# Performance work log

Hardware: AMD Instinct MI355X
Metric: run time of the kernel (lower is better)

## Reference

```python
import jax, jax.numpy as jnp
import numpy as np


def setup_inputs() -> dict:
    key = jax.random.key(0)
    k1, k2, k3, k4 = jax.random.split(key, 4)
    T, H, E, I = 4096, 1024, 8, 3584
    return {
        "hidden_states": jax.random.normal(k1, (T, H), dtype=jnp.float32),
        "gate_w": jax.random.normal(k2, (H, E), dtype=jnp.float32) * 0.02,
        "w1": jax.random.normal(k3, (E, H, I), dtype=jnp.float32) * 0.02,
        "w2": jax.random.normal(k4, (E, I, H), dtype=jnp.float32) * 0.02,
        "top_k": 2,
    }


def reference(hidden_states, gate_w, w1, w2, top_k):
    # Router: logits -> softmax -> top-k -> renormalize (Mixtral / vLLM fused_moe)
    router_logits = hidden_states @ gate_w                    # [T, E]
    probs = jax.nn.softmax(router_logits, axis=-1)
    top_vals, top_idx = jax.lax.top_k(probs, top_k)           # [T, K]
    top_vals = top_vals / jnp.sum(top_vals, axis=-1, keepdims=True)
    E = gate_w.shape[1]
    # Dense per-(token, expert) combine weights, zero for non-selected experts
    dense_w = jnp.sum(jax.nn.one_hot(top_idx, E, dtype=hidden_states.dtype)
                      * top_vals[..., None], axis=1)          # [T, E]
    # Expert MLP: silu(x @ w1[e]) @ w2[e], weighted by routing probs
    act = jax.nn.silu(jnp.einsum('th,ehi->tei', hidden_states, w1))  # [T, E, I]
    act = act * dense_w[:, :, None]
    out = jnp.einsum('tei,eih->th', act, w2)                  # [T, H]
    return out
```

## Files before the change

### kernel.cpp

```cpp
#include <hip/hip_runtime.h>
#include <hip/hip_bf16.h>

#define T_TOK 4096
#define H_DIM 1024
#define E_NUM 8
#define I_DIM 3584
#define NPAIR (T_TOK * 2)
#define MAX_RT 72

#define BM 128
#define BN 128
#define BK 64

typedef __attribute__((ext_vector_type(8))) short bf16x8;
typedef __attribute__((ext_vector_type(4))) float f32x4;
typedef __attribute__((ext_vector_type(8))) unsigned short ushort8_t;
typedef __attribute__((ext_vector_type(4))) unsigned short ushort4_t;

__device__ __forceinline__ unsigned short f2bf(float x) {
  unsigned int u = __float_as_uint(x);
  unsigned int r = (u + 0x7FFFu + ((u >> 16) & 1u)) >> 16;
  return (unsigned short)r;
}

__device__ __forceinline__ void gload16(const void* g, unsigned short* l) {
  __builtin_amdgcn_global_load_lds(
      (const __attribute__((address_space(1))) void*)g,
      (__attribute__((address_space(3))) void*)l, 16, 0, 0);
}

__device__ __forceinline__ void transpose_body(const float* __restrict__ src,
                                               unsigned short* __restrict__ dst,
                                               int R, int C, int e, int c0, int r0,
                                               char* smem) {
  float (*tile)[65] = reinterpret_cast<float (*)[65]>(smem);
  const float* s = src + (size_t)e * R * C;
  unsigned short* d = dst + (size_t)e * R * C;
  const int th = threadIdx.x;
  const int tr = th >> 4;
  const int tc4 = (th & 15) * 4;
#pragma unroll
  for (int it = 0; it < 4; ++it) {
    const int r = it * 16 + tr;
    float4 v = *reinterpret_cast<const float4*>(s + (size_t)(r0 + r) * C + c0 + tc4);
    tile[r][tc4] = v.x; tile[r][tc4 + 1] = v.y; tile[r][tc4 + 2] = v.z; tile[r][tc4 + 3] = v.w;
  }
  __syncthreads();
  const int wc = th >> 3;
  const int wr = (th & 7) * 8;
#pragma unroll
  for (int it = 0; it < 2; ++it) {
    const int c = it * 32 + wc;
    ushort8_t o;
#pragma unroll
    for (int j = 0; j < 8; ++j) o[j] = f2bf(tile[wr + j][c]);
    *reinterpret_cast<ushort8_t*>(d + (size_t)(c0 + c) * R + r0 + wr) = o;
  }
}

__device__ __forceinline__ void router_body(const float* __restrict__ hs,
                                            const float* __restrict__ gw,
                                            unsigned short* __restrict__ hsb,
                                            int* __restrict__ eid, float* __restrict__ wgt,
                                            int* __restrict__ counts, int rbid, char* smem) {
  float* s_gw = reinterpret_cast<float*>(smem);
  int* s_cnt = reinterpret_cast<int*>(smem + 32768);
  const int th = threadIdx.x;
  for (int u = th; u < 2048; u += 256) {
    const f32x4 v = *reinterpret_cast<const f32x4*>(gw + u * 4);
    *reinterpret_cast<f32x4*>(&s_gw[(u ^ ((u >> 3) & 7)) * 4]) = v;
  }
  if (th < E_NUM) s_cnt[th] = 0;
  __syncthreads();

  const int l = th & 63, w = th >> 6;
#pragma unroll 1
  for (int tt = 0; tt < 4; ++tt) {
    const int t = rbid * 16 + w * 4 + tt;
    const float* hrow = hs + (size_t)t * H_DIM;
    unsigned short* brow = hsb + (size_t)t * H_DIM;
    float acc[E_NUM];
#pragma unroll
    for (int e = 0; e < E_NUM; ++e) acc[e] = 0.f;
#pragma unroll
    for (int i = 0; i < 4; ++i) {
      const int h0 = i * 256 + l * 4;
      const f32x4 x = *reinterpret_cast<const f32x4*>(hrow + h0);
      ushort4_t o = { f2bf(x[0]), f2bf(x[1]), f2bf(x[2]), f2bf(x[3]) };
      *reinterpret_cast<ushort4_t*>(brow + h0) = o;
#pragma unroll
      for (int j = 0; j < 4; ++j) {
        const int h = h0 + j;
        const int p0 = (h * 2) ^ ((h >> 2) & 7);
        const f32x4 g0 = *reinterpret_cast<const f32x4*>(&s_gw[p0 * 4]);
        const f32x4 g1 = *reinterpret_cast<const f32x4*>(&s_gw[(p0 ^ 1) * 4]);
        acc[0] += x[j] * g0[0]; acc[1] += x[j] * g0[1];
        acc[2] += x[j] * g0[2]; acc[3] += x[j] * g0[3];
        acc[4] += x[j] * g1[0]; acc[5] += x[j] * g1[1];
        acc[6] += x[j] * g1[2]; acc[7] += x[j] * g1[3];
      }
    }
#pragma unroll
    for (int e = 0; e < E_NUM; ++e) {
#pragma unroll
      for (int off = 1; off < 64; off <<= 1) acc[e] += __shfl_xor(acc[e], off);
    }
    if (l == 0) {
      int i1 = 0;
#pragma unroll
      for (int e = 1; e < E_NUM; ++e) if (acc[e] > acc[i1]) i1 = e;
      int i2 = (i1 == 0) ? 1 : 0;
#pragma unroll
      for (int e = 0; e < E_NUM; ++e) if (e != i1 && acc[e] > acc[i2]) i2 = e;
      const float e2 = __expf(acc[i2] - acc[i1]);
      const float inv = 1.f / (1.f + e2);
      eid[t * 2] = i1;     wgt[t * 2] = inv;
      eid[t * 2 + 1] = i2; wgt[t * 2 + 1] = e2 * inv;
      atomicAdd(&s_cnt[i1], 1);
      atomicAdd(&s_cnt[i2], 1);
    }
  }
  __syncthreads();
  if (th < E_NUM && s_cnt[th] > 0) atomicAdd(&counts[th], s_cnt[th]);
}

__global__ __launch_bounds__(256) void prep_kernel(
    const float* __restrict__ w1, const float* __restrict__ w2,
    const float* __restrict__ hs, const float* __restrict__ gw,
    unsigned short* __restrict__ w1t, unsigned short* __restrict__ w2t,
    unsigned short* __restrict__ hsb,
    int* __restrict__ eid, float* __restrict__ wgt, int* __restrict__ counts) {
  __shared__ char smem[33024];
  const int bid = blockIdx.x;
  if (bid < 256) {
    router_body(hs, gw, hsb, eid, wgt, counts, bid, smem);
    return;
  }
  const int idx = bid - 256;
  const float* src;
  unsigned short* dst;
  int R, C, e, c0, r0;
  if (idx < 3584) {
    e = idx / 448; const int rem = idx % 448;
    R = H_DIM; C = I_DIM; c0 = (rem % 56) * 64; r0 = (rem / 56) * 128;
    src = w1; dst = w1t;
  } else {
    const int i2 = idx - 3584;
    e = i2 / 448; const int rem = i2 % 448;
    R = I_DIM; C = H_DIM; c0 = (rem % 16) * 64; r0 = (rem / 16) * 128;
    src = w2; dst = w2t;
  }
  transpose_body(src, dst, R, C, e, c0, r0, smem);
  __syncthreads();
  transpose_body(src, dst, R, C, e, c0, r0 + 64, smem);
}

__global__ void scatter_kernel(const int* __restrict__ eid, const int* __restrict__ counts,
                               int* __restrict__ fill, int* __restrict__ rowmap,
                               int* __restrict__ posmap) {
  __shared__ int hist[E_NUM], base[E_NUM];
  const int th = threadIdx.x;
  const int p = blockIdx.x * 256 + th;
  if (th < E_NUM) hist[th] = 0;
  __syncthreads();
  const int e = eid[p];
  const int rloc = atomicAdd(&hist[e], 1);
  __syncthreads();
  if (th < E_NUM) base[th] = (hist[th] > 0) ? atomicAdd(&fill[th], hist[th]) : 0;
  __syncthreads();
  int off = 0;
#pragma unroll
  for (int i = 0; i < E_NUM; ++i) off += (i < e) ? counts[i] : 0;
  const int pos = off + base[e] + rloc;
  rowmap[pos] = p;
  posmap[p] = pos;
}

__global__ void combine_kernel(const float* __restrict__ res, const int* __restrict__ posmap,
                               float* __restrict__ out) {
  const int t = blockIdx.x;
  const int th = threadIdx.x;
  const int a = posmap[t * 2];
  const int b = posmap[t * 2 + 1];
  const float4 va = *reinterpret_cast<const float4*>(res + (size_t)a * H_DIM + th * 4);
  const float4 vb = *reinterpret_cast<const float4*>(res + (size_t)b * H_DIM + th * 4);
  float4 o = { va.x + vb.x, va.y + vb.y, va.z + vb.z, va.w + vb.w };
  *reinterpret_cast<float4*>(out + (size_t)t * H_DIM + th * 4) = o;
}

template <int MODE, int NCT>
__launch_bounds__(256, 4)
__global__ void moe_gemm(const unsigned short* __restrict__ hsb,
                         const unsigned short* __restrict__ wt,
                         const unsigned short* __restrict__ act_in,
                         unsigned short* __restrict__ act_out,
                         float* __restrict__ res,
                         const int* __restrict__ counts,
                         const int* __restrict__ rowmap,
                         const float* __restrict__ wgt) {
  constexpr int KD = (MODE == 0) ? H_DIM : I_DIM;
  constexpr int NWG = MAX_RT * NCT;
  constexpr int CHUNK = NWG / 8;

  __shared__ unsigned short As[BM * BK];
  __shared__ unsigned short Bs[BN * BK];
  __shared__ float s_w[BM];

  const int bid = blockIdx.x;
  const int wgid = (bid & 7) * CHUNK + (bid >> 3);
  int rt, ct;
  if (MODE == 0) {
    const int l = wgid % CHUNK;
    const int sg = l / 36;
    const int q = l % 36;
    rt = (wgid / CHUNK) * 9 + q % 9;
    ct = sg * 4 + q / 9;
  } else {
    const int c9 = (wgid / CHUNK) * 9;
    const int l = wgid % CHUNK;
    if (l < 64) {
      const int band = l >> 4, inner = l & 15;
      rt = c9 + band * 2 + (inner & 1);
      ct = inner >> 1;
    } else {
      rt = c9 + 8;
      ct = l - 64;
    }
  }

  int e = -1, loc_rt = 0, off_e = 0, cnt = 0;
  {
    int acc_t = 0, off = 0;
#pragma unroll
    for (int ee = 0; ee < E_NUM; ++ee) {
      const int c = counts[ee];
      const int nt = (c + BM - 1) >> 7;
      if (e < 0 && rt < acc_t + nt) { e = ee; loc_rt = rt - acc_t; off_e = off; cnt = c; }
      acc_t += nt; off += c;
    }
  }
  if (e < 0) return;

  const int cnt_local = min(BM, cnt - loc_rt * BM);
  const int r_base = off_e + loc_rt * BM;
  const int th = threadIdx.x;
  const int lane = th & 63, wid = th >> 6;

  if (MODE == 1 && th < BM) {
    int r = loc_rt * BM + th;
    if (r >= cnt) r = cnt - 1;
    s_w[th] = wgt[rowmap[off_e + r]];
  }

  const int n0 = ct * BN;
  const unsigned short* wbase = wt + (size_t)e * ((size_t)I_DIM * H_DIM) + (size_t)n0 * KD;

  const int srow = lane >> 3;
  const int cg = (lane & 7) ^ srow;
  const char* aptr[4];
  const char* bptr[4];
#pragma unroll
  for (int i = 0; i < 4; ++i) {
    const int r = i * 32 + wid * 8 + srow;
    const int rr = (r < cnt_local) ? r : (cnt_local - 1);
    if (MODE == 0) {
      const int tok = rowmap[off_e + loc_rt * BM + rr] >> 1;
      aptr[i] = (const char*)(hsb + (size_t)tok * H_DIM) + cg * 16;
    } else {
      aptr[i] = (const char*)(act_in + (size_t)(r_base + rr) * I_DIM) + cg * 16;
    }
    bptr[i] = (const char*)(wbase + (size_t)r * KD) + cg * 16;
  }
  unsigned short* dstA[4];
  unsigned short* dstB[4];
#pragma unroll
  for (int i = 0; i < 4; ++i) {
    dstA[i] = &As[(i * 32 + wid * 8) * BK];
    dstB[i] = &Bs[(i * 32 + wid * 8) * BK];
  }

  f32x4 acc[4][4];
#pragma unroll
  for (int m = 0; m < 4; ++m)
#pragma unroll
    for (int n = 0; n < 4; ++n) acc[m][n] = (f32x4){0.f, 0.f, 0.f, 0.f};

  const int wm = (wid >> 1) * 64;
  const int wn = (wid & 1) * 64;
  const int fr = lane & 15;
  const int fq = lane >> 4;
  const int sxor = fr & 7;

  for (int k0 = 0; k0 < KD; k0 += BK) {
    const int kb = k0 * 2;
#pragma unroll
    for (int i = 0; i < 4; ++i) gload16(aptr[i] + kb, dstA[i]);
#pragma unroll
    for (int i = 0; i < 4; ++i) gload16(bptr[i] + kb, dstB[i]);
    __syncthreads();

#pragma unroll
    for (int kk = 0; kk < 2; ++kk) {
      bf16x8 af[4], bf[4];
#pragma unroll
      for (int m = 0; m < 4; ++m)
        af[m] = *reinterpret_cast<const bf16x8*>(
            &As[(wm + m * 16 + fr) * BK + ((kk * 4 + fq) ^ sxor) * 8]);
#pragma unroll
      for (int n = 0; n < 4; ++n)
        bf[n] = *reinterpret_cast<const bf16x8*>(
            &Bs[(wn + n * 16 + fr) * BK + ((kk * 4 + fq) ^ sxor) * 8]);
#pragma unroll
      for (int m = 0; m < 4; ++m)
#pragma unroll
        for (int n = 0; n < 4; ++n)
          acc[m][n] = __builtin_amdgcn_mfma_f32_16x16x32_bf16(af[m], bf[n], acc[m][n], 0, 0, 0);
    }
    __syncthreads();
  }

#pragma unroll
  for (int m = 0; m < 4; ++m) {
    const int row = wm + m * 16 + fq * 4;
#pragma unroll
    for (int n = 0; n < 4; ++n) {
      const int col = wn + n * 16 + fr;
#pragma unroll
      for (int r = 0; r < 4; ++r) {
        const int rw = row + r;
        if (rw < cnt_local) {
          const float x = acc[m][n][r];
          if (MODE == 0) {
            const float s = x / (1.f + __expf(-x));
            act_out[(size_t)(r_base + rw) * I_DIM + n0 + col] = f2bf(s);
          } else {
            res[(size_t)(r_base + rw) * H_DIM + n0 + col] = x * s_w[rw];
          }
        }
      }
    }
  }
}

extern "C" void kernel_launch(void* const* d_in, const int* in_sizes, int n_in,
                              void* d_out, int out_size, void* d_ws, size_t ws_size,
                              hipStream_t stream) {
  const float* hs = (const float*)d_in[0];
  const float* gw = (const float*)d_in[1];
  const float* w1 = (const float*)d_in[2];
  const float* w2 = (const float*)d_in[3];
  float* out = (float*)d_out;

  char* ws = (char*)d_ws;
  const size_t WMAT = (size_t)E_NUM * I_DIM * H_DIM * 2;
  unsigned short* w1t = (unsigned short*)ws;
  unsigned short* w2t = (unsigned short*)(ws + WMAT);
  unsigned short* act = (unsigned short*)(ws + 2 * WMAT);
  unsigned short* hsb = (unsigned short*)(ws + 3 * WMAT);
  float* res = (float*)w1t;
  char* small = ws + 3 * WMAT + (size_t)T_TOK * H_DIM * 2;
  int* eid = (int*)small;
  float* wgt = (float*)(small + NPAIR * 4);
  int* rowmap = (int*)(small + 2 * NPAIR * 4);
  int* posmap = (int*)(small + 3 * NPAIR * 4);
  int* counts = (int*)(small + 4 * NPAIR * 4);
  int* fill = counts + 8;

  hipMemsetAsync(counts, 0, 16 * sizeof(int), stream);

  prep_kernel<<<7424, 256, 0, stream>>>(w1, w2, hs, gw, w1t, w2t, hsb, eid, wgt, counts);
  scatter_kernel<<<NPAIR / 256, 256, 0, stream>>>(eid, counts, fill, rowmap, posmap);

  moe_gemm<0, I_DIM / BN><<<MAX_RT * (I_DIM / BN), 256, 0, stream>>>(
      hsb, w1t, nullptr, act, nullptr, counts, rowmap, wgt);
  moe_gemm<1, H_DIM / BN><<<MAX_RT * (H_DIM / BN), 256, 0, stream>>>(
      hsb, w2t, act, nullptr, res, counts, rowmap, wgt);

  combine_kernel<<<T_TOK, 256, 0, stream>>>(res, posmap, out);
}
```

Measured before the change: 251.8 us.

## Split-K the down-projection GEMM into two partials summed in combine

```diff
diff --git a/kernel.cpp b/kernel.cpp
--- a/kernel.cpp
+++ b/kernel.cpp
@@ -32,8 +32,7 @@
 __device__ __forceinline__ void transpose_body(const float* __restrict__ src,
                                                unsigned short* __restrict__ dst,
                                                int R, int C, int e, int c0, int r0,
-                                               char* smem) {
-  float (*tile)[65] = reinterpret_cast<float (*)[65]>(smem);
+                                               float (*tile)[65]) {
   const float* s = src + (size_t)e * R * C;
   unsigned short* d = dst + (size_t)e * R * C;
   const int th = threadIdx.x;
@@ -62,17 +61,11 @@
                                             const float* __restrict__ gw,
                                             unsigned short* __restrict__ hsb,
                                             int* __restrict__ eid, float* __restrict__ wgt,
-                                            int* __restrict__ counts, int rbid, char* smem) {
-  float* s_gw = reinterpret_cast<float*>(smem);
-  int* s_cnt = reinterpret_cast<int*>(smem + 32768);
-  const int th = threadIdx.x;
-  for (int u = th; u < 2048; u += 256) {
-    const f32x4 v = *reinterpret_cast<const f32x4*>(gw + u * 4);
-    *reinterpret_cast<f32x4*>(&s_gw[(u ^ ((u >> 3) & 7)) * 4]) = v;
-  }
+                                            int* __restrict__ counts, int rbid,
+                                            int* s_cnt) {
+  const int th = threadIdx.x;
   if (th < E_NUM) s_cnt[th] = 0;
   __syncthreads();
-
   const int l = th & 63, w = th >> 6;
 #pragma unroll 1
   for (int tt = 0; tt < 4; ++tt) {
@@ -91,9 +84,8 @@
 #pragma unroll
       for (int j = 0; j < 4; ++j) {
         const int h = h0 + j;
-        const int p0 = (h * 2) ^ ((h >> 2) & 7);
-        const f32x4 g0 = *reinterpret_cast<const f32x4*>(&s_gw[p0 * 4]);
-        const f32x4 g1 = *reinterpret_cast<const f32x4*>(&s_gw[(p0 ^ 1) * 4]);
+        const f32x4 g0 = *reinterpret_cast<const f32x4*>(gw + h * 8);
+        const f32x4 g1 = *reinterpret_cast<const f32x4*>(gw + h * 8 + 4);
         acc[0] += x[j] * g0[0]; acc[1] += x[j] * g0[1];
         acc[2] += x[j] * g0[2]; acc[3] += x[j] * g0[3];
         acc[4] += x[j] * g1[0]; acc[5] += x[j] * g1[1];
@@ -130,10 +122,11 @@
     unsigned short* __restrict__ w1t, unsigned short* __restrict__ w2t,
     unsigned short* __restrict__ hsb,
     int* __restrict__ eid, float* __restrict__ wgt, int* __restrict__ counts) {
-  __shared__ char smem[33024];
+  __shared__ float tile[64][65];
+  __shared__ int s_cnt[E_NUM];
   const int bid = blockIdx.x;
   if (bid < 256) {
-    router_body(hs, gw, hsb, eid, wgt, counts, bid, smem);
+    router_body(hs, gw, hsb, eid, wgt, counts, bid, s_cnt);
     return;
   }
   const int idx = bid - 256;
@@ -150,9 +143,9 @@
     R = I_DIM; C = H_DIM; c0 = (rem % 16) * 64; r0 = (rem / 16) * 128;
     src = w2; dst = w2t;
   }
-  transpose_body(src, dst, R, C, e, c0, r0, smem);
-  __syncthreads();
-  transpose_body(src, dst, R, C, e, c0, r0 + 64, smem);
+  transpose_body(src, dst, R, C, e, c0, r0, tile);
+  __syncthreads();
+  transpose_body(src, dst, R, C, e, c0, r0 + 64, tile);
 }
 
 __global__ void scatter_kernel(const int* __restrict__ eid, const int* __restrict__ counts,
@@ -180,15 +173,19 @@
                                float* __restrict__ out) {
   const int t = blockIdx.x;
   const int th = threadIdx.x;
-  const int a = posmap[t * 2];
-  const int b = posmap[t * 2 + 1];
-  const float4 va = *reinterpret_cast<const float4*>(res + (size_t)a * H_DIM + th * 4);
-  const float4 vb = *reinterpret_cast<const float4*>(res + (size_t)b * H_DIM + th * 4);
-  float4 o = { va.x + vb.x, va.y + vb.y, va.z + vb.z, va.w + vb.w };
+  const size_t a = (size_t)posmap[t * 2] * H_DIM + th * 4;
+  const size_t b = (size_t)posmap[t * 2 + 1] * H_DIM + th * 4;
+  const size_t S = (size_t)NPAIR * H_DIM;
+  const float4 a0 = *reinterpret_cast<const float4*>(res + a);
+  const float4 b0 = *reinterpret_cast<const float4*>(res + b);
+  const float4 a1 = *reinterpret_cast<const float4*>(res + S + a);
+  const float4 b1 = *reinterpret_cast<const float4*>(res + S + b);
+  float4 o = { ((a0.x + a1.x) + (b0.x + b1.x)), ((a0.y + a1.y) + (b0.y + b1.y)),
+               ((a0.z + a1.z) + (b0.z + b1.z)), ((a0.w + a1.w) + (b0.w + b1.w)) };
   *reinterpret_cast<float4*>(out + (size_t)t * H_DIM + th * 4) = o;
 }
 
-template <int MODE, int NCT>
+template <int MODE, int NCT, int KS>
 __launch_bounds__(256, 4)
 __global__ void moe_gemm(const unsigned short* __restrict__ hsb,
                          const unsigned short* __restrict__ wt,
@@ -198,8 +195,9 @@
                          const int* __restrict__ counts,
                          const int* __restrict__ rowmap,
                          const float* __restrict__ wgt) {
-  constexpr int KD = (MODE == 0) ? H_DIM : I_DIM;
-  constexpr int NWG = MAX_RT * NCT;
+  constexpr int KROW = (MODE == 0) ? H_DIM : I_DIM;
+  constexpr int KD = KROW / KS;
+  constexpr int NWG = MAX_RT * NCT * KS;
   constexpr int CHUNK = NWG / 8;
 
   __shared__ unsigned short As[BM * BK];
@@ -208,7 +206,7 @@
 
   const int bid = blockIdx.x;
   const int wgid = (bid & 7) * CHUNK + (bid >> 3);
-  int rt, ct;
+  int rt, ct, ksi = 0;
   if (MODE == 0) {
     const int l = wgid % CHUNK;
     const int sg = l / 36;
@@ -217,7 +215,9 @@
     ct = sg * 4 + q / 9;
   } else {
     const int c9 = (wgid / CHUNK) * 9;
-    const int l = wgid % CHUNK;
+    int l = wgid % CHUNK;
+    ksi = l / (CHUNK / KS);
+    l %= (CHUNK / KS);
     if (l < 64) {
       const int band = l >> 4, inner = l & 15;
       rt = c9 + band * 2 + (inner & 1);
@@ -227,6 +227,7 @@
       ct = l - 64;
     }
   }
+  const int kbase = ksi * KD;
 
   int e = -1, loc_rt = 0, off_e = 0, cnt = 0;
   {
@@ -253,7 +254,8 @@
   }
 
   const int n0 = ct * BN;
-  const unsigned short* wbase = wt + (size_t)e * ((size_t)I_DIM * H_DIM) + (size_t)n0 * KD;
+  const unsigned short* wbase =
+      wt + (size_t)e * ((size_t)I_DIM * H_DIM) + (size_t)n0 * KROW + kbase;
 
   const int srow = lane >> 3;
   const int cg = (lane & 7) ^ srow;
@@ -267,9 +269,9 @@
       const int tok = rowmap[off_e + loc_rt * BM + rr] >> 1;
       aptr[i] = (const char*)(hsb + (size_t)tok * H_DIM) + cg * 16;
     } else {
-      aptr[i] = (const char*)(act_in + (size_t)(r_base + rr) * I_DIM) + cg * 16;
-    }
-    bptr[i] = (const char*)(wbase + (size_t)r * KD) + cg * 16;
+      aptr[i] = (const char*)(act_in + (size_t)(r_base + rr) * I_DIM + kbase) + cg * 16;
+    }
+    bptr[i] = (const char*)(wbase + (size_t)r * KROW) + cg * 16;
   }
   unsigned short* dstA[4];
   unsigned short* dstB[4];
@@ -334,7 +336,8 @@
             const float s = x / (1.f + __expf(-x));
             act_out[(size_t)(r_base + rw) * I_DIM + n0 + col] = f2bf(s);
           } else {
-            res[(size_t)(r_base + rw) * H_DIM + n0 + col] = x * s_w[rw];
+            res[(size_t)ksi * ((size_t)NPAIR * H_DIM) +
+                (size_t)(r_base + rw) * H_DIM + n0 + col] = x * s_w[rw];
           }
         }
       }
@@ -353,9 +356,9 @@
 
   char* ws = (char*)d_ws;
   const size_t WMAT = (size_t)E_NUM * I_DIM * H_DIM * 2;
-  unsigned short* w1t = (unsigned short*)ws;
-  unsigned short* w2t = (unsigned short*)(ws + WMAT);
-  unsigned short* act = (unsigned short*)(ws + 2 * WMAT);
+  unsigned short* w2t = (unsigned short*)ws;
+  unsigned short* act = (unsigned short*)(ws + WMAT);
+  unsigned short* w1t = (unsigned short*)(ws + 2 * WMAT);
   unsigned short* hsb = (unsigned short*)(ws + 3 * WMAT);
   float* res = (float*)w1t;
   char* small = ws + 3 * WMAT + (size_t)T_TOK * H_DIM * 2;
@@ -371,9 +374,9 @@
   prep_kernel<<<7424, 256, 0, stream>>>(w1, w2, hs, gw, w1t, w2t, hsb, eid, wgt, counts);
   scatter_kernel<<<NPAIR / 256, 256, 0, stream>>>(eid, counts, fill, rowmap, posmap);
 
-  moe_gemm<0, I_DIM / BN><<<MAX_RT * (I_DIM / BN), 256, 0, stream>>>(
+  moe_gemm<0, I_DIM / BN, 1><<<MAX_RT * (I_DIM / BN), 256, 0, stream>>>(
       hsb, w1t, nullptr, act, nullptr, counts, rowmap, wgt);
-  moe_gemm<1, H_DIM / BN><<<MAX_RT * (H_DIM / BN), 256, 0, stream>>>(
+  moe_gemm<1, H_DIM / BN, 2><<<MAX_RT * (H_DIM / BN) * 2, 256, 0, stream>>>(
       hsb, w2t, act, nullptr, res, counts, rowmap, wgt);
 
   combine_kernel<<<T_TOK, 256, 0, stream>>>(res, posmap, out);
```

After: 260.2 us. 1.03x slower.
